# Kernel tuning notes

Hardware: AMD Instinct MI355X
Metric: run time of the kernel (lower is better)

## Reference

```python
import jax, jax.numpy as jnp
import numpy as np
from jax import lax

D_MODEL = 1024
N_HEADS = 16
KERNEL = 3
STRIDE = 1
PAD = 1
BATCH = 32
SEQ = D_MODEL  # required by the module's reshape: seq_len must equal d_model


def setup_inputs() -> dict:
    key = jax.random.key(0)
    k1, k2, k3, k4, k5, k6 = jax.random.split(key, 6)
    query_sequences = jax.random.normal(k1, (BATCH, SEQ, D_MODEL), dtype=jnp.float32)
    key_sequences = jax.random.normal(k2, (BATCH, SEQ, D_MODEL), dtype=jnp.float32)
    value_sequences = jax.random.normal(k3, (BATCH, SEQ, D_MODEL), dtype=jnp.float32)
    key_value_sequence_lengths = jax.random.randint(k4, (BATCH,), 0, SEQ).astype(jnp.int64)
    # nn.Linear(d_model, n_heads*kernel_size) params (stored as (in, out) for x @ W)
    scale = 1.0 / np.sqrt(D_MODEL)
    Wq = jax.random.uniform(k5, (D_MODEL, N_HEADS * KERNEL), minval=-scale, maxval=scale, dtype=jnp.float32)
    bq = jax.random.uniform(k6, (N_HEADS * KERNEL,), minval=-scale, maxval=scale, dtype=jnp.float32)
    return {
        "query_sequences": query_sequences,
        "key_sequences": key_sequences,
        "value_sequences": value_sequences,
        "key_value_sequence_lengths": key_value_sequence_lengths,
        "Wq": Wq,
        "bq": bq,
    }


def reference(query_sequences, key_sequences, value_sequences, key_value_sequence_lengths, Wq, bq):
    B, S, D = query_sequences.shape
    # per-batch dynamic conv kernels from queries: (B, S, H*K) -> (B*H, D, K)
    # (valid because S == D, mirroring the torch .view)
    qk = jnp.einsum('bsd,df->bsf', query_sequences, Wq) + bq
    kernels = qk.reshape(B * N_HEADS, D, KERNEL)
    # keys as a single grouped-conv input: (1, B*D, S)
    keys = jnp.transpose(key_sequences, (0, 2, 1)).reshape(1, B * D, S)
    # grouped conv1d with groups = batch_size (each group: in=D, out=N_HEADS)
    out = lax.conv_general_dilated(
        keys, kernels,
        window_strides=(STRIDE,),
        padding=[(PAD, PAD)],
        dimension_numbers=('NCH', 'OIH', 'NCH'),
        feature_group_count=B,
    )
    return out.reshape(B, N_HEADS, S)
```

## Files before the change

### kernel.cpp

```cpp
#include <hip/hip_runtime.h>
#include <hip/hip_bf16.h>
#include <stdint.h>

typedef __attribute__((ext_vector_type(8))) short bf16x8;
typedef __attribute__((ext_vector_type(4))) float f32x4;

__device__ __forceinline__ short f2bf(float x) {
    __hip_bfloat16 h = __float2bfloat16(x);
    return __builtin_bit_cast(short, h);
}

__device__ __forceinline__ bf16x8 pack8(f32x4 a, f32x4 b) {
    bf16x8 r;
    r[0] = f2bf(a[0]); r[1] = f2bf(a[1]); r[2] = f2bf(a[2]); r[3] = f2bf(a[3]);
    r[4] = f2bf(b[0]); r[5] = f2bf(b[1]); r[6] = f2bf(b[2]); r[7] = f2bf(b[3]);
    return r;
}

__global__ __launch_bounds__(256) void prep_wfrag(const float* __restrict__ Wq,
                                                  short* __restrict__ wfrag) {
    int idx = blockIdx.x * 256 + threadIdx.x;
    int j    = idx & 7;
    int lane = (idx >> 3) & 63;
    int grp  = idx >> 9;
    int nf   = grp % 3;
    int ks   = grp / 3;
    int k = ks * 32 + ((lane >> 4) << 3) + j;
    int n = nf * 16 + (lane & 15);
    wfrag[idx] = f2bf(Wq[k * 48 + n]);
}

__global__ __launch_bounds__(256) void qk_gemm(const float* __restrict__ Q,
                                               const short* __restrict__ wfrag,
                                               const float* __restrict__ bq,
                                               short* __restrict__ wgtA) {
    const int l  = threadIdx.x & 63;
    const int w  = threadIdx.x >> 6;
    const int lr = l & 15;
    const int lk = l >> 4;
    const int row0 = blockIdx.x * 64 + w * 16;

    f32x4 acc[3];
    acc[0] = (f32x4){0.f, 0.f, 0.f, 0.f};
    acc[1] = acc[0];
    acc[2] = acc[0];

    const float* qbase = Q + (size_t)(row0 + lr) * 1024 + lk * 8;

    #pragma unroll 4
    for (int ks = 0; ks < 32; ++ks) {
        const float* p = qbase + ks * 32;
        f32x4 q0 = *(const f32x4*)p;
        f32x4 q1 = *(const f32x4*)(p + 4);
        bf16x8 a = pack8(q0, q1);
        const bf16x8* wp = (const bf16x8*)(wfrag + (size_t)ks * 1536 + l * 8);
        acc[0] = __builtin_amdgcn_mfma_f32_16x16x32_bf16(a, wp[0],   acc[0], 0, 0, 0);
        acc[1] = __builtin_amdgcn_mfma_f32_16x16x32_bf16(a, wp[64],  acc[1], 0, 0, 0);
        acc[2] = __builtin_amdgcn_mfma_f32_16x16x32_bf16(a, wp[128], acc[2], 0, 0, 0);
    }

    #pragma unroll
    for (int nf = 0; nf < 3; ++nf) {
        int n = nf * 16 + lr;
        float bias = bq[n];
        int t  = n / 3;
        int kk = n - t * 3;
        #pragma unroll
        for (int r = 0; r < 4; ++r) {
            int row = row0 + lk * 4 + r;
            int b   = row >> 10;
            int h   = (row >> 6) & 15;
            int sp  = row & 63;
            int dg  = sp * 2 + (t >> 3);
            int j   = t & 7;
            wgtA[(((size_t)(b * 3 + kk) * 128 + dg) << 7) + h * 8 + j] = f2bf(acc[nf][r] + bias);
        }
    }
}

__global__ __launch_bounds__(256, 4) void conv_mfma(const float* __restrict__ Key,
                                                    const short* __restrict__ wgtA,
                                                    float* __restrict__ out) {
    __shared__ short klds[4][2][18][64];
    __shared__ float red[2][16][17];
    const int blk = blockIdx.x;
    const int st  = blk & 31;
    const int b   = blk >> 5;
    const int tid = threadIdx.x;
    const int l   = tid & 63;
    const int w   = tid >> 6;
    const int lr  = l & 15;
    const int lk  = l >> 4;
    const int ss  = w & 1;
    const int dh  = w >> 1;
    const int sbase = (st << 5) + (ss << 4);

    const int row16 = l >> 2;
    const int cg    = l & 3;
    const int rowX  = 16 + (l >> 2);
    const int srowA = sbase - 1 + row16;
    const int srowX = sbase + 15 + (l >> 2);
    const bool okA  = (srowA >= 0);
    const bool okX  = (l < 8) && (srowX < 1024);

    const float* keyW = Key + ((size_t)b << 20) + (dh << 9);
    const f32x4* pA = (const f32x4*)(keyW + (size_t)(okA ? srowA : 0) * 1024 + cg * 16);
    const f32x4* pX = (const f32x4*)(keyW + (size_t)(okX ? srowX : 0) * 1024 + cg * 16);

    char* ldsW = (char*)&klds[w][0][0][0];
    const int swzA = (row16 & 7) << 4;
    const int swzX = (rowX & 7) << 4;

    const f32x4 z4 = (f32x4){0.f, 0.f, 0.f, 0.f};
    f32x4 mA[4], mX[4];

    #define LOADS(t) do {                                            \
        const int o = (t) * 16;                                      \
        mA[0] = okA ? pA[o]     : z4;  mA[1] = okA ? pA[o + 1] : z4; \
        mA[2] = okA ? pA[o + 2] : z4;  mA[3] = okA ? pA[o + 3] : z4; \
        mX[0] = okX ? pX[o]     : z4;  mX[1] = okX ? pX[o + 1] : z4; \
        mX[2] = okX ? pX[o + 2] : z4;  mX[3] = okX ? pX[o + 3] : z4; \
    } while (0)

    #define WRITES(buf) do {                                                  \
        char* bb = ldsW + (buf) * 2304;                                       \
        *(bf16x8*)(bb + row16 * 128 + (((cg << 5))      ^ swzA)) = pack8(mA[0], mA[1]); \
        *(bf16x8*)(bb + row16 * 128 + (((cg << 5) + 16) ^ swzA)) = pack8(mA[2], mA[3]); \
        if (l < 8) {                                                          \
            *(bf16x8*)(bb + rowX * 128 + (((cg << 5))      ^ swzX)) = pack8(mX[0], mX[1]); \
            *(bf16x8*)(bb + rowX * 128 + (((cg << 5) + 16) ^ swzX)) = pack8(mX[2], mX[3]); \
        }                                                                     \
    } while (0)

    const short* wgtW = wgtA + (((size_t)b * 384 + (dh << 6) + lk) << 7) + lr * 8;

    f32x4 acc = z4;

    LOADS(0);
    WRITES(0);
    LOADS(1);

    #pragma unroll
    for (int t = 0; t < 8; ++t) {
        const int buf = t & 1;
        #pragma unroll
        for (int k = 0; k < 3; ++k) {
            const int row = lr + k;
            const char* rb = ldsW + buf * 2304 + row * 128;
            const int sw = (row & 7) << 4;
            #pragma unroll
            for (int kk = 0; kk < 2; ++kk) {
                bf16x8 kv = *(const bf16x8*)(rb + (((kk << 6) + (lk << 4)) ^ sw));
                bf16x8 a  = *(const bf16x8*)(wgtW + k * 16384 + t * 1024 + kk * 512);
                acc = __builtin_amdgcn_mfma_f32_16x16x32_bf16(a, kv, acc, 0, 0, 0);
            }
        }
        if (t < 7) {
            WRITES(buf ^ 1);
            if (t < 6) LOADS(t + 2);
        }
    }
    #undef LOADS
    #undef WRITES

    if (dh == 1) {
        #pragma unroll
        for (int r4 = 0; r4 < 4; ++r4) red[ss][lk * 4 + r4][lr] = acc[r4];
    }
    __syncthreads();
    if (dh == 0) {
        const int s = sbase + lr;
        #pragma unroll
        for (int r4 = 0; r4 < 4; ++r4) {
            int h = lk * 4 + r4;
            out[(((b << 4) + h) << 10) + s] = acc[r4] + red[ss][h][lr];
        }
    }
}

extern "C" void kernel_launch(void* const* d_in, const int* in_sizes, int n_in,
                              void* d_out, int out_size, void* d_ws, size_t ws_size,
                              hipStream_t stream) {
    const float* Q  = (const float*)d_in[0];
    const float* K  = (const float*)d_in[1];
    const float* Wq = (const float*)d_in[4];
    const float* bq = (const float*)d_in[5];
    float* outp = (float*)d_out;

    short* wfrag = (short*)d_ws;
    short* wgtA  = (short*)((char*)d_ws + 98304);

    hipLaunchKernelGGL(prep_wfrag, dim3(192),  dim3(256), 0, stream, Wq, wfrag);
    hipLaunchKernelGGL(qk_gemm,    dim3(512),  dim3(256), 0, stream, Q, wfrag, bq, wgtA);
    hipLaunchKernelGGL(conv_mfma,  dim3(1024), dim3(256), 0, stream, K, wgtA, outp);
}
```

Baseline: 68.86 us.

## Stage key tiles via direct global-to-LDS loads with 4-deep pipelined buffering

Replaces the per-wave register-staged fp32→bf16 key loads with a single wave issuing global_load_lds copies of raw fp32 key rows into a 4-slot shared ring buffer, three stages ahead, with swizzled addresses. All waves then read fp32 from LDS, convert to bf16 at MFMA time, and synchronise through explicit vmcnt waits and barriers. Edge rows are zero-filled for the first and last tiles, weight fragments are double-buffered in registers, and block indices are remapped to spread batches across XCDs. This is meant to cut register pressure and the VGPR round trip for key staging, at the cost of doubling LDS traffic (fp32 instead of bf16), adding two barriers per step, and relying on hand-counted vmcnt values that are fragile.

```diff
diff --git a/kernel.cpp b/kernel.cpp
--- a/kernel.cpp
+++ b/kernel.cpp
@@ -16,6 +16,10 @@
     r[4] = f2bf(b[0]); r[5] = f2bf(b[1]); r[6] = f2bf(b[2]); r[7] = f2bf(b[3]);
     return r;
 }
+
+#define GLDS(gp, lp) __builtin_amdgcn_global_load_lds( \
+    (const __attribute__((address_space(1))) void*)(gp), \
+    (__attribute__((address_space(3))) void*)(lp), 16, 0, 0)
 
 __global__ __launch_bounds__(256) void prep_wfrag(const float* __restrict__ Wq,
                                                   short* __restrict__ wfrag) {
@@ -81,9 +85,9 @@
 __global__ __launch_bounds__(256, 4) void conv_mfma(const float* __restrict__ Key,
                                                     const short* __restrict__ wgtA,
                                                     float* __restrict__ out) {
-    __shared__ short klds[4][2][18][64];
+    __shared__ char stage[4 * 9216];
     __shared__ float red[2][16][17];
-    const int blk = blockIdx.x;
+    const int blk = (blockIdx.x & 7) * 128 + (blockIdx.x >> 3);
     const int st  = blk & 31;
     const int b   = blk >> 5;
     const int tid = threadIdx.x;
@@ -93,75 +97,82 @@
     const int lk  = l >> 4;
     const int ss  = w & 1;
     const int dh  = w >> 1;
-    const int sbase = (st << 5) + (ss << 4);
-
-    const int row16 = l >> 2;
-    const int cg    = l & 3;
-    const int rowX  = 16 + (l >> 2);
-    const int srowA = sbase - 1 + row16;
-    const int srowX = sbase + 15 + (l >> 2);
-    const bool okA  = (srowA >= 0);
-    const bool okX  = (l < 8) && (srowX < 1024);
-
-    const float* keyW = Key + ((size_t)b << 20) + (dh << 9);
-    const f32x4* pA = (const f32x4*)(keyW + (size_t)(okA ? srowA : 0) * 1024 + cg * 16);
-    const f32x4* pX = (const f32x4*)(keyW + (size_t)(okX ? srowX : 0) * 1024 + cg * 16);
-
-    char* ldsW = (char*)&klds[w][0][0][0];
-    const int swzA = (row16 & 7) << 4;
-    const int swzX = (rowX & 7) << 4;
-
-    const f32x4 z4 = (f32x4){0.f, 0.f, 0.f, 0.f};
-    f32x4 mA[4], mX[4];
-
-    #define LOADS(t) do {                                            \
-        const int o = (t) * 16;                                      \
-        mA[0] = okA ? pA[o]     : z4;  mA[1] = okA ? pA[o + 1] : z4; \
-        mA[2] = okA ? pA[o + 2] : z4;  mA[3] = okA ? pA[o + 3] : z4; \
-        mX[0] = okX ? pX[o]     : z4;  mX[1] = okX ? pX[o + 1] : z4; \
-        mX[2] = okX ? pX[o + 2] : z4;  mX[3] = okX ? pX[o + 3] : z4; \
-    } while (0)
-
-    #define WRITES(buf) do {                                                  \
-        char* bb = ldsW + (buf) * 2304;                                       \
-        *(bf16x8*)(bb + row16 * 128 + (((cg << 5))      ^ swzA)) = pack8(mA[0], mA[1]); \
-        *(bf16x8*)(bb + row16 * 128 + (((cg << 5) + 16) ^ swzA)) = pack8(mA[2], mA[3]); \
-        if (l < 8) {                                                          \
-            *(bf16x8*)(bb + rowX * 128 + (((cg << 5))      ^ swzX)) = pack8(mX[0], mX[1]); \
-            *(bf16x8*)(bb + rowX * 128 + (((cg << 5) + 16) ^ swzX)) = pack8(mX[2], mX[3]); \
-        }                                                                     \
-    } while (0)
+    const int s0  = st << 5;
+
+    const char* gaddr[9];
+    {
+        const char* keyB = (const char*)(Key + ((size_t)b << 20));
+        int cb = (l & 15) << 4;
+        #pragma unroll
+        for (int i = 0; i < 9; ++i) {
+            int grow = i * 4 + (l >> 4);
+            int srow = s0 - 1 + grow;
+            srow = srow < 0 ? 0 : (srow > 1023 ? 1023 : srow);
+            int gb   = cb ^ ((grow & 7) << 4);
+            int colb = gb + ((gb >> 7) * 1920);
+            gaddr[i] = keyB + (size_t)srow * 4096 + colb;
+        }
+    }
 
     const short* wgtW = wgtA + (((size_t)b * 384 + (dh << 6) + lk) << 7) + lr * 8;
-
-    f32x4 acc = z4;
-
-    LOADS(0);
-    WRITES(0);
-    LOADS(1);
-
-    #pragma unroll
-    for (int t = 0; t < 8; ++t) {
-        const int buf = t & 1;
-        #pragma unroll
-        for (int k = 0; k < 3; ++k) {
-            const int row = lr + k;
-            const char* rb = ldsW + buf * 2304 + row * 128;
-            const int sw = (row & 7) << 4;
-            #pragma unroll
-            for (int kk = 0; kk < 2; ++kk) {
-                bf16x8 kv = *(const bf16x8*)(rb + (((kk << 6) + (lk << 4)) ^ sw));
-                bf16x8 a  = *(const bf16x8*)(wgtW + k * 16384 + t * 1024 + kk * 512);
-                acc = __builtin_amdgcn_mfma_f32_16x16x32_bf16(a, kv, acc, 0, 0, 0);
-            }
-        }
-        if (t < 7) {
-            WRITES(buf ^ 1);
-            if (t < 6) LOADS(t + 2);
-        }
-    }
-    #undef LOADS
-    #undef WRITES
+    bf16x8 aw0[3], aw1[3];
+    f32x4 acc = (f32x4){0.f, 0.f, 0.f, 0.f};
+
+    #define ALOADV(arr, tt) do{ _Pragma("unroll") \
+        for (int k3 = 0; k3 < 3; ++k3) \
+            arr[k3] = *(const bf16x8*)(wgtW + k3 * 16384 + (tt) * 512); }while(0)
+
+    #define STAGEV(tt) do{ char* bb_ = stage + ((tt) & 3) * 9216; _Pragma("unroll") \
+        for (int i9 = 0; i9 < 9; ++i9) GLDS(gaddr[i9] + (tt) * 128, bb_ + i9 * 1024); }while(0)
+
+    #define ZFIX(tt) do{ \
+        if (st == 0  && l < 16) *(f32x4*)(stage + ((tt)&3)*9216 + (l<<4)) = (f32x4){0.f,0.f,0.f,0.f}; \
+        if (st == 31 && l < 16) *(f32x4*)(stage + ((tt)&3)*9216 + 33*256 + (l<<4)) = (f32x4){0.f,0.f,0.f,0.f}; \
+        if (st == 0 || st == 31) asm volatile("s_waitcnt lgkmcnt(0)" ::: "memory"); }while(0)
+
+    #define COMP(tt) do{ \
+        const char* bb_ = stage + ((tt) & 3) * 9216; \
+        _Pragma("unroll") for (int k3 = 0; k3 < 3; ++k3) { \
+            int row_ = ss * 16 + lr + k3; \
+            const char* rb_ = bb_ + row_ * 256; \
+            int sw_ = (row_ & 7) << 4; \
+            int x_  = (dh << 7) + (lk << 5); \
+            f32x4 v0_ = *(const f32x4*)(rb_ + ((x_) ^ sw_)); \
+            f32x4 v1_ = *(const f32x4*)(rb_ + ((x_ + 16) ^ sw_)); \
+            bf16x8 a_ = ((tt) & 1) ? aw1[k3] : aw0[k3]; \
+            acc = __builtin_amdgcn_mfma_f32_16x16x32_bf16(a_, pack8(v0_, v1_), acc, 0, 0, 0); \
+        } }while(0)
+
+    #define STEP(tt, NW0, NWX) do{ \
+        if ((tt) < 15) { if ((tt) & 1) ALOADV(aw0, (tt)+1); else ALOADV(aw1, (tt)+1); } \
+        if (w == 0) { \
+            if ((tt) < 13) STAGEV((tt) + 3); \
+            asm volatile("s_waitcnt vmcnt(" NW0 ")" ::: "memory"); \
+            ZFIX(tt); \
+        } else { \
+            asm volatile("s_waitcnt vmcnt(" NWX ")" ::: "memory"); \
+        } \
+        __builtin_amdgcn_s_barrier(); \
+        asm volatile("" ::: "memory"); \
+        COMP(tt); \
+        asm volatile("" ::: "memory"); \
+        __builtin_amdgcn_s_barrier(); }while(0)
+
+    if (w == 0) { STAGEV(0); STAGEV(1); STAGEV(2); }
+    ALOADV(aw0, 0);
+
+    STEP(0,  "21", "3");  STEP(1,  "21", "3");  STEP(2,  "21", "3");
+    STEP(3,  "21", "3");  STEP(4,  "21", "3");  STEP(5,  "21", "3");
+    STEP(6,  "21", "3");  STEP(7,  "21", "3");  STEP(8,  "21", "3");
+    STEP(9,  "21", "3");  STEP(10, "21", "3");  STEP(11, "21", "3");
+    STEP(12, "21", "3");  STEP(13, "12", "3");  STEP(14, "3",  "3");
+    STEP(15, "0",  "0");
+
+    #undef ALOADV
+    #undef STAGEV
+    #undef ZFIX
+    #undef COMP
+    #undef STEP
 
     if (dh == 1) {
         #pragma unroll
@@ -169,7 +180,7 @@
     }
     __syncthreads();
     if (dh == 0) {
-        const int s = sbase + lr;
+        const int s = s0 + ss * 16 + lr;
         #pragma unroll
         for (int r4 = 0; r4 < 4; ++r4) {
             int h = lk * 4 + r4;
```

After: 60.21 us. -12.6%, faster.

## Load conv key taps directly from global memory, dropping LDS staging

Applied to the files above, without the earlier changes.

The conv kernel stops staging key rows in LDS. Each lane now loads its three shifted key rows (s-1, s, s+1) straight from global memory into registers and packs them to bf16 as MFMA B operands, with a two-deep register double-buffer for keys and weights. This removes the LDS writes and reads and the swizzle arithmetic. In exchange each key row is fetched three times from global memory or cache instead of once, and register pressure rises. The block index is also remapped so consecutive workgroups spread across batches, which may change L2 and channel locality.

```diff
diff --git a/kernel.cpp b/kernel.cpp
--- a/kernel.cpp
+++ b/kernel.cpp
@@ -81,9 +81,8 @@
 __global__ __launch_bounds__(256, 4) void conv_mfma(const float* __restrict__ Key,
                                                     const short* __restrict__ wgtA,
                                                     float* __restrict__ out) {
-    __shared__ short klds[4][2][18][64];
     __shared__ float red[2][16][17];
-    const int blk = blockIdx.x;
+    const int blk = (blockIdx.x & 7) * 128 + (blockIdx.x >> 3);
     const int st  = blk & 31;
     const int b   = blk >> 5;
     const int tid = threadIdx.x;
@@ -93,75 +92,52 @@
     const int lk  = l >> 4;
     const int ss  = w & 1;
     const int dh  = w >> 1;
-    const int sbase = (st << 5) + (ss << 4);
+    const int s   = (st << 5) + (ss << 4) + lr;
 
-    const int row16 = l >> 2;
-    const int cg    = l & 3;
-    const int rowX  = 16 + (l >> 2);
-    const int srowA = sbase - 1 + row16;
-    const int srowX = sbase + 15 + (l >> 2);
-    const bool okA  = (srowA >= 0);
-    const bool okX  = (l < 8) && (srowX < 1024);
-
-    const float* keyW = Key + ((size_t)b << 20) + (dh << 9);
-    const f32x4* pA = (const f32x4*)(keyW + (size_t)(okA ? srowA : 0) * 1024 + cg * 16);
-    const f32x4* pX = (const f32x4*)(keyW + (size_t)(okX ? srowX : 0) * 1024 + cg * 16);
-
-    char* ldsW = (char*)&klds[w][0][0][0];
-    const int swzA = (row16 & 7) << 4;
-    const int swzX = (rowX & 7) << 4;
+    const bool ok0 = (s > 0);
+    const bool ok2 = (s < 1023);
+    const float* keyB = Key + ((size_t)b << 20) + (dh << 9) + (lk << 3);
+    const f32x4* pk0 = (const f32x4*)(keyB + (size_t)(ok0 ? s - 1 : 0) * 1024);
+    const f32x4* pk1 = (const f32x4*)(keyB + (size_t)s * 1024);
+    const f32x4* pk2 = (const f32x4*)(keyB + (size_t)(ok2 ? s + 1 : 1023) * 1024);
+    const short* wgtW = wgtA + (((size_t)b * 384 + (dh << 6) + lk) << 7) + lr * 8;
 
     const f32x4 z4 = (f32x4){0.f, 0.f, 0.f, 0.f};
-    f32x4 mA[4], mX[4];
-
-    #define LOADS(t) do {                                            \
-        const int o = (t) * 16;                                      \
-        mA[0] = okA ? pA[o]     : z4;  mA[1] = okA ? pA[o + 1] : z4; \
-        mA[2] = okA ? pA[o + 2] : z4;  mA[3] = okA ? pA[o + 3] : z4; \
-        mX[0] = okX ? pX[o]     : z4;  mX[1] = okX ? pX[o + 1] : z4; \
-        mX[2] = okX ? pX[o + 2] : z4;  mX[3] = okX ? pX[o + 3] : z4; \
-    } while (0)
-
-    #define WRITES(buf) do {                                                  \
-        char* bb = ldsW + (buf) * 2304;                                       \
-        *(bf16x8*)(bb + row16 * 128 + (((cg << 5))      ^ swzA)) = pack8(mA[0], mA[1]); \
-        *(bf16x8*)(bb + row16 * 128 + (((cg << 5) + 16) ^ swzA)) = pack8(mA[2], mA[3]); \
-        if (l < 8) {                                                          \
-            *(bf16x8*)(bb + rowX * 128 + (((cg << 5))      ^ swzX)) = pack8(mX[0], mX[1]); \
-            *(bf16x8*)(bb + rowX * 128 + (((cg << 5) + 16) ^ swzX)) = pack8(mX[2], mX[3]); \
-        }                                                                     \
-    } while (0)
-
-    const short* wgtW = wgtA + (((size_t)b * 384 + (dh << 6) + lk) << 7) + lr * 8;
-
+    f32x4 a00, a01, a10, a11, a20, a21;
+    f32x4 b00, b01, b10, b11, b20, b21;
+    bf16x8 wa0, wa1, wa2, wb0, wb1, wb2;
     f32x4 acc = z4;
 
-    LOADS(0);
-    WRITES(0);
-    LOADS(1);
+    #define KLOAD(S, tt) do{ \
+        S##00 = pk0[(tt) * 8];  S##01 = pk0[(tt) * 8 + 1]; \
+        S##10 = pk1[(tt) * 8];  S##11 = pk1[(tt) * 8 + 1]; \
+        S##20 = pk2[(tt) * 8];  S##21 = pk2[(tt) * 8 + 1]; }while(0)
+
+    #define WLOAD(S, tt) do{ \
+        w##S##0 = *(const bf16x8*)(wgtW +         (tt) * 512); \
+        w##S##1 = *(const bf16x8*)(wgtW + 16384 + (tt) * 512); \
+        w##S##2 = *(const bf16x8*)(wgtW + 32768 + (tt) * 512); }while(0)
+
+    #define CONSUME(S) do{ \
+        f32x4 t00 = ok0 ? S##00 : z4, t01 = ok0 ? S##01 : z4; \
+        f32x4 t20 = ok2 ? S##20 : z4, t21 = ok2 ? S##21 : z4; \
+        acc = __builtin_amdgcn_mfma_f32_16x16x32_bf16(w##S##0, pack8(t00, t01),     acc, 0, 0, 0); \
+        acc = __builtin_amdgcn_mfma_f32_16x16x32_bf16(w##S##1, pack8(S##10, S##11), acc, 0, 0, 0); \
+        acc = __builtin_amdgcn_mfma_f32_16x16x32_bf16(w##S##2, pack8(t20, t21),     acc, 0, 0, 0); }while(0)
+
+    KLOAD(a, 0);  WLOAD(a, 0);
+    KLOAD(b, 1);  WLOAD(b, 1);
 
     #pragma unroll
-    for (int t = 0; t < 8; ++t) {
-        const int buf = t & 1;
-        #pragma unroll
-        for (int k = 0; k < 3; ++k) {
-            const int row = lr + k;
-            const char* rb = ldsW + buf * 2304 + row * 128;
-            const int sw = (row & 7) << 4;
-            #pragma unroll
-            for (int kk = 0; kk < 2; ++kk) {
-                bf16x8 kv = *(const bf16x8*)(rb + (((kk << 6) + (lk << 4)) ^ sw));
-                bf16x8 a  = *(const bf16x8*)(wgtW + k * 16384 + t * 1024 + kk * 512);
-                acc = __builtin_amdgcn_mfma_f32_16x16x32_bf16(a, kv, acc, 0, 0, 0);
-            }
-        }
-        if (t < 7) {
-            WRITES(buf ^ 1);
-            if (t < 6) LOADS(t + 2);
-        }
+    for (int t = 0; t < 16; t += 2) {
+        CONSUME(a);
+        if (t + 2 < 16) { KLOAD(a, t + 2); WLOAD(a, t + 2); }
+        CONSUME(b);
+        if (t + 3 < 16) { KLOAD(b, t + 3); WLOAD(b, t + 3); }
     }
-    #undef LOADS
-    #undef WRITES
+    #undef KLOAD
+    #undef WLOAD
+    #undef CONSUME
 
     if (dh == 1) {
         #pragma unroll
@@ -169,7 +145,6 @@
     }
     __syncthreads();
     if (dh == 0) {
-        const int s = sbase + lr;
         #pragma unroll
         for (int r4 = 0; r4 < 4; ++r4) {
             int h = lk * 4 + r4;
```

After: 90.73 us. 31.8% more time.
